# Optimization experiments

Measured on AMD Instinct MI355X. Metric: run time of the kernel, lower is better.

Reference implementation:

```python
import jax, jax.numpy as jnp
import numpy as np

NUM_CLASSES = 21
IOU_THRESH = 0.5
NEG_POS_RATIO = 3
VAR0, VAR1 = 0.1, 0.2


def point_form(priors):
    # (cx,cy,w,h) -> (xmin,ymin,xmax,ymax)
    return jnp.concatenate([priors[:, :2] - priors[:, 2:] / 2,
                            priors[:, :2] + priors[:, 2:] / 2], axis=-1)


def jaccard(box_a, box_b):
    # box_a: [n,4] point form, box_b: [N,4] point form -> [n,N]
    max_xy = jnp.minimum(box_a[:, None, 2:], box_b[None, :, 2:])
    min_xy = jnp.maximum(box_a[:, None, :2], box_b[None, :, :2])
    inter = jnp.prod(jnp.clip(max_xy - min_xy, 0.0, None), axis=-1)
    area_a = jnp.prod(box_a[:, 2:] - box_a[:, :2], axis=-1)[:, None]
    area_b = jnp.prod(box_b[:, 2:] - box_b[:, :2], axis=-1)[None, :]
    return inter / (area_a + area_b - inter)


def encode(matched, priors):
    # matched: [N,4] point form, priors: [N,4] center form
    g_cxcy = ((matched[:, :2] + matched[:, 2:]) / 2 - priors[:, :2]) / (VAR0 * priors[:, 2:])
    g_wh = jnp.log((matched[:, 2:] - matched[:, :2]) / priors[:, 2:]) / VAR1
    return jnp.concatenate([g_cxcy, g_wh], axis=-1)


def match_one(truths, labels, priors):
    # truths: [n_obj,4], labels: [n_obj], priors: [N,4] center form
    ov = jaccard(truths, point_form(priors))          # [n_obj, N]
    best_prior_idx = jnp.argmax(ov, axis=1)           # [n_obj]
    best_truth_overlap = jnp.max(ov, axis=0)          # [N]
    best_truth_idx = jnp.argmax(ov, axis=0)           # [N]
    best_truth_overlap = best_truth_overlap.at[best_prior_idx].set(2.0)
    def body(j, bti):
        return bti.at[best_prior_idx[j]].set(j)
    best_truth_idx = jax.lax.fori_loop(0, truths.shape[0], body, best_truth_idx)
    matched = truths[best_truth_idx]                  # [N,4]
    conf = labels[best_truth_idx].astype(jnp.int32) + 1
    conf = jnp.where(best_truth_overlap < IOU_THRESH, 0, conf)
    return encode(matched, priors), conf


def smooth_l1(x):
    ax = jnp.abs(x)
    return jnp.where(ax < 1.0, 0.5 * x * x, ax - 0.5)


def setup_inputs() -> dict:
    key = jax.random.key(0)
    k1, k2, k3, k4, k5, k6, k7 = jax.random.split(key, 7)
    B, N, n_obj = 128, 8732, 16
    loc_data = jax.random.normal(k1, (B, N, 4), jnp.float32)
    conf_data = jax.random.normal(k2, (B, N, NUM_CLASSES), jnp.float32)
    # valid ground-truth boxes in [0,1], point form, plus class label in [0,20)
    mins = jax.random.uniform(k3, (B, n_obj, 2)) * 0.6
    sizes = jax.random.uniform(k4, (B, n_obj, 2)) * 0.35 + 0.05
    labels = jax.random.randint(k5, (B, n_obj), 0, NUM_CLASSES - 1).astype(jnp.float32)
    targets = jnp.concatenate([mins, mins + sizes, labels[..., None]], axis=-1)
    # priors in center form with positive w,h
    centers = jax.random.uniform(k6, (N, 2))
    wh = jax.random.uniform(k7, (N, 2)) * 0.5 + 0.05
    priors = jnp.concatenate([centers, wh], axis=-1).astype(jnp.float32)
    return {"loc_data": loc_data, "conf_data": conf_data, "targets": targets, "priors": priors}


def _forward(loc_data, conf_data, targets, priors):
    B, N = loc_data.shape[0], loc_data.shape[1]
    truths, labels = targets[:, :, :4], targets[:, :, 4]
    target_loc, target_conf = jax.vmap(match_one, in_axes=(0, 0, None))(truths, labels, priors)
    pos = target_conf > 0                             # [B,N]
    # localization: smooth-L1 summed over positive priors
    loss_l = jnp.sum(smooth_l1(loc_data - target_loc) * pos[..., None].astype(loc_data.dtype))
    # per-prior CE surrogate: logsumexp - logit[target]
    lse = jax.nn.logsumexp(conf_data, axis=-1)        # [B,N]
    gathered = jnp.take_along_axis(conf_data, target_conf[..., None], axis=-1)[..., 0]
    loss_c_all = lse - gathered                       # [B,N]
    # hard negative mining via double argsort ranking (positives excluded)
    lc = jnp.where(pos, 0.0, loss_c_all)
    loss_idx = jnp.argsort(-lc, axis=1)
    idx_rank = jnp.argsort(loss_idx, axis=1)
    num_pos = jnp.sum(pos.astype(jnp.int32), axis=1, keepdims=True)   # [B,1]
    num_neg = jnp.minimum(NEG_POS_RATIO * num_pos, N - 1)
    neg = idx_rank < num_neg
    sel = pos | neg
    loss_c = jnp.sum(jnp.where(sel, loss_c_all, 0.0))
    n_total = jnp.sum(num_pos).astype(loc_data.dtype)
    return loss_l / n_total, loss_c / n_total


def reference(loc_data, conf_data, targets, priors):
    return _forward(loc_data, conf_data, targets, priors)
```

## Files before the change

kernel.cpp:

```cpp
#include <hip/hip_runtime.h>
#include <cstdint>
#include <cstddef>

#define HB1 4096
#define HB2 2048
#define CMAX 21
#define IOU_T 0.5f

__device__ __forceinline__ float sl1(float x) {
    float ax = fabsf(x);
    return ax < 1.0f ? 0.5f * x * x : ax - 0.5f;
}

__global__ __launch_bounds__(256) void kA_best_prior(
    const float* __restrict__ targets, const float* __restrict__ priors,
    float* __restrict__ bpi_val, int* __restrict__ bpi_idx,
    int* __restrict__ num_pos_g, float* __restrict__ accB_g,
    float* __restrict__ acc_g, unsigned* __restrict__ done_g,
    int N, int NOBJ, int SLICES, int CHUNK, int B)
{
    const int s = blockIdx.x, b = blockIdx.y, t = threadIdx.x;
    __shared__ float tb[16 * 4];
    __shared__ float ta[16];
    __shared__ float wv[4 * 16];
    __shared__ int   wi[4 * 16];

    if (s == 0 && b == 0) {
        for (int q = t; q < B; q += 256) num_pos_g[q] = 0;
        for (int q = t; q < 2 * B; q += 256) accB_g[q] = 0.f;
        if (t < 4) acc_g[t] = 0.f;
        if (t == 0) *done_g = 0u;
    }

    if (t < 16) {
        if (t < NOBJ) {
            const float* tr = targets + ((size_t)b * NOBJ + t) * 5;
            float x0 = tr[0], y0 = tr[1], x1 = tr[2], y1 = tr[3];
            tb[t * 4 + 0] = x0; tb[t * 4 + 1] = y0;
            tb[t * 4 + 2] = x1; tb[t * 4 + 3] = y1;
            ta[t] = (x1 - x0) * (y1 - y0);
        } else {
            tb[t * 4 + 0] = 0.f; tb[t * 4 + 1] = 0.f;
            tb[t * 4 + 2] = 0.f; tb[t * 4 + 3] = 0.f;
            ta[t] = 0.f;
        }
    }
    __syncthreads();

    float bv[16]; int bi[16];
#pragma unroll
    for (int j = 0; j < 16; j++) { bv[j] = -1.0f; bi[j] = 0x7fffffff; }

    const int start = s * CHUNK;
    const int end = min(start + CHUNK, N);
    for (int i = start + t; i < end; i += 256) {
        float4 p = ((const float4*)priors)[i];
        float bx0 = p.x - p.z * 0.5f, by0 = p.y - p.w * 0.5f;
        float bx1 = p.x + p.z * 0.5f, by1 = p.y + p.w * 0.5f;
        float ab = (bx1 - bx0) * (by1 - by0);
#pragma unroll
        for (int j = 0; j < 16; j++) {
            float iw = fminf(tb[j * 4 + 2], bx1) - fmaxf(tb[j * 4 + 0], bx0);
            float ih = fminf(tb[j * 4 + 3], by1) - fmaxf(tb[j * 4 + 1], by0);
            iw = fmaxf(iw, 0.f); ih = fmaxf(ih, 0.f);
            float inter = iw * ih;
            float iou = inter / (ta[j] + ab - inter);
            if (iou > bv[j] || (iou == bv[j] && i < bi[j])) { bv[j] = iou; bi[j] = i; }
        }
    }

#pragma unroll
    for (int off = 32; off >= 1; off >>= 1) {
#pragma unroll
        for (int j = 0; j < 16; j++) {
            float v2 = __shfl_down(bv[j], off, 64);
            int   i2 = __shfl_down(bi[j], off, 64);
            if (v2 > bv[j] || (v2 == bv[j] && i2 < bi[j])) { bv[j] = v2; bi[j] = i2; }
        }
    }
    const int wid = t >> 6, lane = t & 63;
    if (lane == 0) {
#pragma unroll
        for (int j = 0; j < 16; j++) { wv[wid * 16 + j] = bv[j]; wi[wid * 16 + j] = bi[j]; }
    }
    __syncthreads();
    if (t < 16) {
        float v = wv[t]; int idx = wi[t];
#pragma unroll
        for (int w = 1; w < 4; w++) {
            float v2 = wv[w * 16 + t]; int i2 = wi[w * 16 + t];
            if (v2 > v || (v2 == v && i2 < idx)) { v = v2; idx = i2; }
        }
        if (t < NOBJ) {
            int o = (b * SLICES + s) * 16 + t;
            bpi_val[o] = v;
            bpi_idx[o] = idx;
        }
    }
}

#define IOU_STEP(j) { \
    float4 tj = tb4[j]; \
    float taj = (tj.z - tj.x) * (tj.w - tj.y); \
    float iw = fminf(tj.z, bx1) - fmaxf(tj.x, bx0); \
    float ih = fminf(tj.w, by1) - fmaxf(tj.y, by0); \
    iw = fmaxf(iw, 0.f); ih = fmaxf(ih, 0.f); \
    float inter = iw * ih; \
    float iou = inter * __builtin_amdgcn_rcpf(taj + ab - inter); \
    if (iou > bto) { bto = iou; bti = (j); } }

__global__ __launch_bounds__(256, 4) void kB_main(
    const float* __restrict__ loc, const float* __restrict__ conf,
    const float* __restrict__ targets, const float* __restrict__ priors,
    const float* __restrict__ bpi_val, const int* __restrict__ bpi_idx,
    float* __restrict__ lc_out, int* __restrict__ num_pos, float* __restrict__ accB,
    int N, int NOBJ, int SLICES, int BPB)
{
    const int g = blockIdx.x;
    const int b = g / BPB;
    const int j0 = g % BPB;
    const int t = threadIdx.x;
    const int wid = t >> 6, lane = t & 63;

    __shared__ __align__(16) float tb[16 * 4];
    __shared__ float tl[16];
    __shared__ __align__(16) int bpi_s[16];
    __shared__ float wred[4 * 3];

    if (t < 16) {
        if (t < NOBJ) {
            const float* tr = targets + ((size_t)b * NOBJ + t) * 5;
            tb[t * 4 + 0] = tr[0]; tb[t * 4 + 1] = tr[1];
            tb[t * 4 + 2] = tr[2]; tb[t * 4 + 3] = tr[3];
            tl[t] = tr[4];
            float bv = -1.f; int bi = 0x7fffffff;
            for (int s2 = 0; s2 < SLICES; s2++) {
                int o = (b * SLICES + s2) * 16 + t;
                float v = bpi_val[o]; int idx = bpi_idx[o];
                if (v > bv || (v == bv && idx < bi)) { bv = v; bi = idx; }
            }
            bpi_s[t] = bi;
        } else {
            tb[t * 4 + 0] = 0.f; tb[t * 4 + 1] = 0.f; tb[t * 4 + 2] = 0.f; tb[t * 4 + 3] = 0.f;
            tl[t] = 0.f; bpi_s[t] = -1;
        }
    }
    __syncthreads();

    const float* confB = conf + (size_t)b * N * CMAX;
    const float* locB  = loc + (size_t)b * N * 4;

    float ll = 0.f, plc = 0.f, np = 0.f;

    const int stride = BPB * 256;
    for (int i = j0 * 256 + t; i < N; i += stride) {
        float4 pp  = ((const float4*)priors)[i];
        float4 myl = ((const float4*)locB)[i];
        const float* cr = confB + (size_t)i * CMAX;
        float c[CMAX];
#pragma unroll
        for (int q = 0; q < CMAX; q++) c[q] = cr[q];

        float bx0 = pp.x - pp.z * 0.5f, by0 = pp.y - pp.w * 0.5f;
        float bx1 = pp.x + pp.z * 0.5f, by1 = pp.y + pp.w * 0.5f;
        float ab = (bx1 - bx0) * (by1 - by0);
        float bto = -1.f; int bti = 0;
        const float4* tb4 = (const float4*)tb;
        if (NOBJ == 16) {
#pragma unroll
            for (int j = 0; j < 16; j++) IOU_STEP(j);
        } else {
            for (int j = 0; j < NOBJ; j++) IOU_STEP(j);
        }
        const int4* bp4 = (const int4*)bpi_s;
#pragma unroll
        for (int jj = 0; jj < 4; jj++) {
            int4 q = bp4[jj];
            if (q.x == i) { bto = 2.0f; bti = jj * 4 + 0; }
            if (q.y == i) { bto = 2.0f; bti = jj * 4 + 1; }
            if (q.z == i) { bto = 2.0f; bti = jj * 4 + 2; }
            if (q.w == i) { bto = 2.0f; bti = jj * 4 + 3; }
        }
        bool pos = !(bto < IOU_T);
        if (pos) {
            float4 tj = tb4[bti];
            float rz = __builtin_amdgcn_rcpf(pp.z);
            float rw = __builtin_amdgcn_rcpf(pp.w);
            float gcx = ((tj.x + tj.z) * 0.5f - pp.x) * (10.0f * rz);
            float gcy = ((tj.y + tj.w) * 0.5f - pp.y) * (10.0f * rw);
            float gw = __logf((tj.z - tj.x) * rz) * 5.0f;
            float gh = __logf((tj.w - tj.y) * rw) * 5.0f;
            ll += sl1(myl.x - gcx) + sl1(myl.y - gcy) + sl1(myl.z - gw) + sl1(myl.w - gh);
            np += 1.f;
        }
        int cf = pos ? ((int)tl[bti] + 1) : 0;

        float m = c[0];
#pragma unroll
        for (int q = 1; q < CMAX; q++) m = fmaxf(m, c[q]);
        float ssum = 0.f;
#pragma unroll
        for (int q = 0; q < CMAX; q++) ssum += __expf(c[q] - m);
        float gath = c[0];
#pragma unroll
        for (int q = 1; q < CMAX; q++) gath = (q == cf) ? c[q] : gath;
        float lse = m + __logf(ssum);
        float lossc = lse - gath;
        if (pos) plc += lossc;
        float lcv = pos ? 0.f : lossc;
        lcv = fmaxf(lcv, 0.f);
        lc_out[(size_t)b * N + i] = lcv;
    }

#pragma unroll
    for (int off = 32; off >= 1; off >>= 1) {
        ll  += __shfl_down(ll, off, 64);
        plc += __shfl_down(plc, off, 64);
        np  += __shfl_down(np, off, 64);
    }
    if (lane == 0) { wred[wid * 3 + 0] = ll; wred[wid * 3 + 1] = plc; wred[wid * 3 + 2] = np; }
    __syncthreads();
    if (t == 0) {
        float a0 = 0.f, a1 = 0.f, a2 = 0.f;
#pragma unroll
        for (int w = 0; w < 4; w++) { a0 += wred[w * 3 + 0]; a1 += wred[w * 3 + 1]; a2 += wred[w * 3 + 2]; }
        atomicAdd(&accB[b * 2 + 0], a0);
        atomicAdd(&accB[b * 2 + 1], a1);
        atomicAdd(&num_pos[b], (int)a2);
    }
}

__device__ __forceinline__ void wave_sufscan(int& c, float& s, int lane) {
#pragma unroll
    for (int off = 1; off < 64; off <<= 1) {
        int c2 = __shfl_down(c, off, 64);
        float s2 = __shfl_down(s, off, 64);
        if (lane + off < 64) { c += c2; s += s2; }
    }
}

__global__ __launch_bounds__(1024) void kC_topk(
    const float* __restrict__ lc, const int* __restrict__ num_pos,
    const float* __restrict__ accB,
    float* __restrict__ acc, unsigned* __restrict__ done_ctr,
    float* __restrict__ out, int N, int B)
{
    const int b = blockIdx.x, t = threadIdx.x;
    const int NT = 1024;
    const int wid = t >> 6, lane = t & 63;
    __shared__ __align__(16) int   cnt[HB1];
    __shared__ __align__(16) float sm[HB1];
    __shared__ int   wc[16];
    __shared__ float ws[16];
    __shared__ int s_strad, s_krem;
    __shared__ float s_above;
    __shared__ int s_last;
    __shared__ float wsum[16], wsA[16], wsB[16];

    const int k = min(3 * num_pos[b], N - 1);
    const float* lcb = lc + (size_t)b * N;
    float total = 0.f;

    if (k > 0) {
        ((int4*)cnt)[t] = make_int4(0, 0, 0, 0);
        ((float4*)sm)[t] = make_float4(0.f, 0.f, 0.f, 0.f);
        __syncthreads();
        const int n4 = N >> 2;
        const float4* lcb4 = (const float4*)lcb;
        for (int i = t; i < n4; i += NT) {
            float4 v = lcb4[i];
            { unsigned u = __float_as_uint(v.x) >> 19; atomicAdd(&cnt[u], 1); atomicAdd(&sm[u], v.x); }
            { unsigned u = __float_as_uint(v.y) >> 19; atomicAdd(&cnt[u], 1); atomicAdd(&sm[u], v.y); }
            { unsigned u = __float_as_uint(v.z) >> 19; atomicAdd(&cnt[u], 1); atomicAdd(&sm[u], v.z); }
            { unsigned u = __float_as_uint(v.w) >> 19; atomicAdd(&cnt[u], 1); atomicAdd(&sm[u], v.w); }
        }
        for (int i = (n4 << 2) + t; i < N; i += NT) {
            float v = lcb[i];
            unsigned u = __float_as_uint(v) >> 19;
            atomicAdd(&cnt[u], 1); atomicAdd(&sm[u], v);
        }
        __syncthreads();
        {
            int4  cv = ((const int4*)cnt)[t];
            float4 sv = ((const float4*)sm)[t];
            int   ci = cv.x + cv.y + cv.z + cv.w;
            float si = sv.x + sv.y + sv.z + sv.w;
            wave_sufscan(ci, si, lane);
            if (lane == 0) { wc[wid] = ci; ws[wid] = si; }
            __syncthreads();
            int cab = 0; float sab = 0.f;
            for (int w = wid + 1; w < 16; w++) { cab += wc[w]; sab += ws[w]; }
            int   i0c = ci + cab;          float f0 = si + sab;
            int   i1c = i0c - cv.x;        float f1 = f0 - sv.x;
            int   i2c = i1c - cv.y;        float f2 = f1 - sv.y;
            int   i3c = i2c - cv.z;        float f3 = f2 - sv.z;
            int   i4c = i3c - cv.w;
            if (i1c < k && k <= i0c) { s_strad = 4 * t + 0; s_krem = k - i1c; s_above = f1; }
            if (i2c < k && k <= i1c) { s_strad = 4 * t + 1; s_krem = k - i2c; s_above = f2; }
            if (i3c < k && k <= i2c) { s_strad = 4 * t + 2; s_krem = k - i3c; s_above = f3; }
            if (i4c < k && k <= i3c) { s_strad = 4 * t + 3; s_krem = k - i4c; s_above = f3 - sv.w; }
        }
        __syncthreads();
        const int s1 = s_strad, k2 = s_krem;
        total += s_above;

        __syncthreads();
        ((int2*)cnt)[t] = make_int2(0, 0);
        ((float2*)sm)[t] = make_float2(0.f, 0.f);
        __syncthreads();
        for (int i = t; i < N; i += NT) {
            float v = lcb[i];
            unsigned u = __float_as_uint(v);
            if ((int)(u >> 19) == s1) {
                int q = (int)((u >> 8) & 0x7FF);
                atomicAdd(&cnt[q], 1); atomicAdd(&sm[q], v);
            }
        }
        __syncthreads();
        {
            int2  cv = ((const int2*)cnt)[t];
            float2 sv = ((const float2*)sm)[t];
            int   ci = cv.x + cv.y;
            float si = sv.x + sv.y;
            wave_sufscan(ci, si, lane);
            if (lane == 0) { wc[wid] = ci; ws[wid] = si; }
            __syncthreads();
            int cab = 0; float sab = 0.f;
            for (int w = wid + 1; w < 16; w++) { cab += wc[w]; sab += ws[w]; }
            int   i0c = ci + cab;       float f0 = si + sab;
            int   i1c = i0c - cv.x;     float f1 = f0 - sv.x;
            int   i2c = i1c - cv.y;
            if (i1c < k2 && k2 <= i0c) { s_strad = 2 * t + 0; s_krem = k2 - i1c; s_above = f1; }
            if (i2c < k2 && k2 <= i1c) { s_strad = 2 * t + 1; s_krem = k2 - i2c; s_above = f1 - sv.y; }
        }
        __syncthreads();
        const int s2 = s_strad, krem = s_krem;
        total += s_above;
        float tval = __uint_as_float((((unsigned)s1) << 19) | (((unsigned)s2) << 8));
        total += (float)krem * tval;
    }

    if (t == 0) {
        if (k > 0) atomicAdd(&acc[1], total);
        __threadfence();
        unsigned old = atomicAdd(done_ctr, 1u);
        s_last = (old == (unsigned)gridDim.x - 1u) ? 1 : 0;
    }
    __syncthreads();
    if (s_last) {
        __threadfence();
        float vn = 0.f, va = 0.f, vb = 0.f;
        for (int q = t; q < B; q += NT) {
            vn += (float)num_pos[q];
            va += accB[q * 2 + 0];
            vb += accB[q * 2 + 1];
        }
#pragma unroll
        for (int off = 32; off >= 1; off >>= 1) {
            vn += __shfl_down(vn, off, 64);
            va += __shfl_down(va, off, 64);
            vb += __shfl_down(vb, off, 64);
        }
        if (lane == 0) { wsum[wid] = vn; wsA[wid] = va; wsB[wid] = vb; }
        __syncthreads();
        if (t == 0) {
            float n = 0.f, a = 0.f, bsum = 0.f;
#pragma unroll
            for (int w = 0; w < 16; w++) { n += wsum[w]; a += wsA[w]; bsum += wsB[w]; }
            float l2 = atomicAdd(&acc[1], 0.0f);
            out[0] = a / n;
            out[1] = (bsum + l2) / n;
        }
    }
}

extern "C" void kernel_launch(void* const* d_in, const int* in_sizes, int n_in,
                              void* d_out, int out_size, void* d_ws, size_t ws_size,
                              hipStream_t stream)
{
    const float* loc     = (const float*)d_in[0];
    const float* conf    = (const float*)d_in[1];
    const float* targets = (const float*)d_in[2];
    const float* priors  = (const float*)d_in[3];
    float* out = (float*)d_out;

    const int N = in_sizes[3] / 4;
    const int BN = in_sizes[0] / 4;
    const int B = BN / N;
    const int NOBJ = in_sizes[2] / (B * 5);
    const int SLICES = 8;
    const int CHUNK = (N + SLICES - 1) / SLICES;
    const int BPB = 12;

    char* w = (char*)d_ws;
    float*    lc_ws   = (float*)w;                         size_t off = (size_t)BN * 4;
    float*    bpi_val = (float*)(w + off);                 off += (size_t)B * SLICES * 16 * 4;
    int*      bpi_idx = (int*)(w + off);                   off += (size_t)B * SLICES * 16 * 4;
    int*      num_pos = (int*)(w + off);                   off += (size_t)B * 4;
    float*    accB    = (float*)(w + off);                 off += (size_t)B * 2 * 4;
    float*    acc     = (float*)(w + off);                 off += 16;
    unsigned* done    = (unsigned*)(w + off);              off += 16;

    dim3 gA(SLICES, B);
    kA_best_prior<<<gA, 256, 0, stream>>>(targets, priors, bpi_val, bpi_idx,
                                          num_pos, accB, acc, done, N, NOBJ, SLICES, CHUNK, B);

    kB_main<<<B * BPB, 256, 0, stream>>>(loc, conf, targets, priors, bpi_val, bpi_idx,
                                         lc_ws, num_pos, accB, N, NOBJ, SLICES, BPB);

    kC_topk<<<B, 1024, 0, stream>>>(lc_ws, num_pos, accB, acc, done, out, N, B);
}
```

Baseline: 269.2 us.

## Stage conf tiles through LDS with coalesced float4 loads and register double-buffering

The main kernel now loads each 256-prior tile of class logits as contiguous float4 vectors into registers, writes them to shared memory, and has each thread read its own row from there. Previously each thread read its 21-float row with strided scalar global loads. The next-but-one tile is prefetched into a second register set while the current tile is processed, so global latency overlaps with compute. Blocks per batch drop from 12 to 8 and the occupancy hint drops to 3, which adds register and LDS pressure. The generic NOBJ path is removed, so the kernel now assumes 16 objects.

Result: faster. 230.7 us (-14.3%).

```diff
diff --git a/kernel.cpp b/kernel.cpp
--- a/kernel.cpp
+++ b/kernel.cpp
@@ -109,12 +109,94 @@
     float iou = inter * __builtin_amdgcn_rcpf(taj + ab - inter); \
     if (iou > bto) { bto = iou; bti = (j); } }
 
-__global__ __launch_bounds__(256, 4) void kB_main(
+#define STAGE(PFX, xx) { \
+    int i0s = (xx) * 256; \
+    int rows_s = min(256, N - i0s); \
+    int nf4s = (rows_s * CMAX) >> 2; \
+    const float4* s4 = (const float4*)(confB + (size_t)i0s * CMAX); \
+    if (t + 0    < nf4s) PFX##0 = s4[t + 0]; \
+    if (t + 256  < nf4s) PFX##1 = s4[t + 256]; \
+    if (t + 512  < nf4s) PFX##2 = s4[t + 512]; \
+    if (t + 768  < nf4s) PFX##3 = s4[t + 768]; \
+    if (t + 1024 < nf4s) PFX##4 = s4[t + 1024]; \
+    if (t + 1280 < nf4s) PFX##5 = s4[t + 1280]; \
+    if (t < rows_s) { \
+        PFX##pr = ((const float4*)priors)[i0s + t]; \
+        PFX##ld = ((const float4*)locB)[i0s + t]; } }
+
+#define PROC_TILE(PFX) { \
+    const int i0 = x * 256; \
+    const int rows = min(256, N - i0); \
+    const int nf4 = (rows * CMAX) >> 2; \
+    asm volatile("" ::: "memory"); \
+    __builtin_amdgcn_s_barrier();                  \
+    asm volatile("" ::: "memory"); \
+    float4 myp = PFX##pr, myl = PFX##ld;           \
+    float4* bp4f = (float4*)buf; \
+    if (t + 0    < nf4) bp4f[t + 0]    = PFX##0;   \
+    if (t + 256  < nf4) bp4f[t + 256]  = PFX##1; \
+    if (t + 512  < nf4) bp4f[t + 512]  = PFX##2; \
+    if (t + 768  < nf4) bp4f[t + 768]  = PFX##3; \
+    if (t + 1024 < nf4) bp4f[t + 1024] = PFX##4; \
+    if (t + 1280 < nf4) bp4f[t + 1280] = PFX##5; \
+    asm volatile("s_waitcnt lgkmcnt(0)" ::: "memory");   \
+    __builtin_amdgcn_s_barrier();                  \
+    asm volatile("" ::: "memory"); \
+    { int xpre = x + 2 * BPB; if (xpre < TPB) STAGE(PFX, xpre); } \
+    if (t < rows) { \
+        const int i = i0 + t; \
+        float4 pp = myp; \
+        float bx0 = pp.x - pp.z * 0.5f, by0 = pp.y - pp.w * 0.5f; \
+        float bx1 = pp.x + pp.z * 0.5f, by1 = pp.y + pp.w * 0.5f; \
+        float ab = (bx1 - bx0) * (by1 - by0); \
+        float bto = -1.f; int bti = 0; \
+        const float4* tb4 = (const float4*)tb; \
+        _Pragma("unroll") \
+        for (int j = 0; j < 16; j++) IOU_STEP(j); \
+        const int4* bp4 = (const int4*)bpi_s; \
+        _Pragma("unroll") \
+        for (int jj = 0; jj < 4; jj++) { \
+            int4 q = bp4[jj]; \
+            if (q.x == i) { bto = 2.0f; bti = jj * 4 + 0; } \
+            if (q.y == i) { bto = 2.0f; bti = jj * 4 + 1; } \
+            if (q.z == i) { bto = 2.0f; bti = jj * 4 + 2; } \
+            if (q.w == i) { bto = 2.0f; bti = jj * 4 + 3; } \
+        } \
+        bool pos = !(bto < IOU_T); \
+        if (pos) { \
+            float4 tj = tb4[bti]; \
+            float rz = __builtin_amdgcn_rcpf(pp.z); \
+            float rw = __builtin_amdgcn_rcpf(pp.w); \
+            float gcx = ((tj.x + tj.z) * 0.5f - pp.x) * (10.0f * rz); \
+            float gcy = ((tj.y + tj.w) * 0.5f - pp.y) * (10.0f * rw); \
+            float gw = __logf((tj.z - tj.x) * rz) * 5.0f; \
+            float gh = __logf((tj.w - tj.y) * rw) * 5.0f; \
+            ll += sl1(myl.x - gcx) + sl1(myl.y - gcy) + sl1(myl.z - gw) + sl1(myl.w - gh); \
+            np += 1.f; \
+        } \
+        int cf = pos ? ((int)tl[bti] + 1) : 0; \
+        const float* cr = buf + t * CMAX; \
+        float m = cr[0]; \
+        _Pragma("unroll") \
+        for (int c = 1; c < CMAX; c++) m = fmaxf(m, cr[c]); \
+        float ssum = 0.f; \
+        _Pragma("unroll") \
+        for (int c = 0; c < CMAX; c++) ssum += __expf(cr[c] - m); \
+        float lse = m + __logf(ssum); \
+        float lossc = lse - cr[cf]; \
+        if (pos) plc += lossc; \
+        float lcv = pos ? 0.f : lossc; \
+        lcv = fmaxf(lcv, 0.f); \
+        lc_out[(size_t)b * N + i] = lcv; \
+    } \
+    x += BPB; }
+
+__global__ __launch_bounds__(256, 3) void kB_main(
     const float* __restrict__ loc, const float* __restrict__ conf,
     const float* __restrict__ targets, const float* __restrict__ priors,
     const float* __restrict__ bpi_val, const int* __restrict__ bpi_idx,
     float* __restrict__ lc_out, int* __restrict__ num_pos, float* __restrict__ accB,
-    int N, int NOBJ, int SLICES, int BPB)
+    int N, int NOBJ, int SLICES, int TPB, int BPB)
 {
     const int g = blockIdx.x;
     const int b = g / BPB;
@@ -122,6 +204,7 @@
     const int t = threadIdx.x;
     const int wid = t >> 6, lane = t & 63;
 
+    __shared__ __align__(16) float buf[256 * CMAX];
     __shared__ __align__(16) float tb[16 * 4];
     __shared__ float tl[16];
     __shared__ __align__(16) int bpi_s[16];
@@ -150,66 +233,18 @@
     const float* confB = conf + (size_t)b * N * CMAX;
     const float* locB  = loc + (size_t)b * N * 4;
 
+    float4 a0, a1, a2, a3, a4, a5, apr, ald;
+    float4 b0, b1, b2, b3, b4, b5, bpr, bld;
+
     float ll = 0.f, plc = 0.f, np = 0.f;
-
-    const int stride = BPB * 256;
-    for (int i = j0 * 256 + t; i < N; i += stride) {
-        float4 pp  = ((const float4*)priors)[i];
-        float4 myl = ((const float4*)locB)[i];
-        const float* cr = confB + (size_t)i * CMAX;
-        float c[CMAX];
-#pragma unroll
-        for (int q = 0; q < CMAX; q++) c[q] = cr[q];
-
-        float bx0 = pp.x - pp.z * 0.5f, by0 = pp.y - pp.w * 0.5f;
-        float bx1 = pp.x + pp.z * 0.5f, by1 = pp.y + pp.w * 0.5f;
-        float ab = (bx1 - bx0) * (by1 - by0);
-        float bto = -1.f; int bti = 0;
-        const float4* tb4 = (const float4*)tb;
-        if (NOBJ == 16) {
-#pragma unroll
-            for (int j = 0; j < 16; j++) IOU_STEP(j);
-        } else {
-            for (int j = 0; j < NOBJ; j++) IOU_STEP(j);
-        }
-        const int4* bp4 = (const int4*)bpi_s;
-#pragma unroll
-        for (int jj = 0; jj < 4; jj++) {
-            int4 q = bp4[jj];
-            if (q.x == i) { bto = 2.0f; bti = jj * 4 + 0; }
-            if (q.y == i) { bto = 2.0f; bti = jj * 4 + 1; }
-            if (q.z == i) { bto = 2.0f; bti = jj * 4 + 2; }
-            if (q.w == i) { bto = 2.0f; bti = jj * 4 + 3; }
-        }
-        bool pos = !(bto < IOU_T);
-        if (pos) {
-            float4 tj = tb4[bti];
-            float rz = __builtin_amdgcn_rcpf(pp.z);
-            float rw = __builtin_amdgcn_rcpf(pp.w);
-            float gcx = ((tj.x + tj.z) * 0.5f - pp.x) * (10.0f * rz);
-            float gcy = ((tj.y + tj.w) * 0.5f - pp.y) * (10.0f * rw);
-            float gw = __logf((tj.z - tj.x) * rz) * 5.0f;
-            float gh = __logf((tj.w - tj.y) * rw) * 5.0f;
-            ll += sl1(myl.x - gcx) + sl1(myl.y - gcy) + sl1(myl.z - gw) + sl1(myl.w - gh);
-            np += 1.f;
-        }
-        int cf = pos ? ((int)tl[bti] + 1) : 0;
-
-        float m = c[0];
-#pragma unroll
-        for (int q = 1; q < CMAX; q++) m = fmaxf(m, c[q]);
-        float ssum = 0.f;
-#pragma unroll
-        for (int q = 0; q < CMAX; q++) ssum += __expf(c[q] - m);
-        float gath = c[0];
-#pragma unroll
-        for (int q = 1; q < CMAX; q++) gath = (q == cf) ? c[q] : gath;
-        float lse = m + __logf(ssum);
-        float lossc = lse - gath;
-        if (pos) plc += lossc;
-        float lcv = pos ? 0.f : lossc;
-        lcv = fmaxf(lcv, 0.f);
-        lc_out[(size_t)b * N + i] = lcv;
+    int x = j0;
+    if (x < TPB)       STAGE(a, x);
+    if (x + BPB < TPB) STAGE(b, x + BPB);
+
+    while (x < TPB) {
+        PROC_TILE(a)
+        if (x >= TPB) break;
+        PROC_TILE(b)
     }
 
 #pragma unroll
@@ -221,12 +256,12 @@
     if (lane == 0) { wred[wid * 3 + 0] = ll; wred[wid * 3 + 1] = plc; wred[wid * 3 + 2] = np; }
     __syncthreads();
     if (t == 0) {
-        float a0 = 0.f, a1 = 0.f, a2 = 0.f;
-#pragma unroll
-        for (int w = 0; w < 4; w++) { a0 += wred[w * 3 + 0]; a1 += wred[w * 3 + 1]; a2 += wred[w * 3 + 2]; }
-        atomicAdd(&accB[b * 2 + 0], a0);
-        atomicAdd(&accB[b * 2 + 1], a1);
-        atomicAdd(&num_pos[b], (int)a2);
+        float a0r = 0.f, a1r = 0.f, a2r = 0.f;
+#pragma unroll
+        for (int w = 0; w < 4; w++) { a0r += wred[w * 3 + 0]; a1r += wred[w * 3 + 1]; a2r += wred[w * 3 + 2]; }
+        atomicAdd(&accB[b * 2 + 0], a0r);
+        atomicAdd(&accB[b * 2 + 1], a1r);
+        atomicAdd(&num_pos[b], (int)a2r);
     }
 }
 
@@ -390,7 +425,8 @@
     const int NOBJ = in_sizes[2] / (B * 5);
     const int SLICES = 8;
     const int CHUNK = (N + SLICES - 1) / SLICES;
-    const int BPB = 12;
+    const int TPB = (N + 255) / 256;
+    const int BPB = 8;
 
     char* w = (char*)d_ws;
     float*    lc_ws   = (float*)w;                         size_t off = (size_t)BN * 4;
@@ -406,7 +442,7 @@
                                           num_pos, accB, acc, done, N, NOBJ, SLICES, CHUNK, B);
 
     kB_main<<<B * BPB, 256, 0, stream>>>(loc, conf, targets, priors, bpi_val, bpi_idx,
-                                         lc_ws, num_pos, accB, N, NOBJ, SLICES, BPB);
+                                         lc_ws, num_pos, accB, N, NOBJ, SLICES, TPB, BPB);
 
     kC_topk<<<B, 1024, 0, stream>>>(lc_ws, num_pos, accB, acc, done, out, N, B);
 }
```

## Double-buffer conf/loc/prior tiles into LDS via global_load_lds in single-wave blocks

Applied to the files above, without the earlier changes.

The main matching and loss kernel now runs one wave per block and streams 64-prior chunks of conf, priors and loc directly into LDS with global_load_lds. It double-buffers them, waiting on vmcnt so the next chunk's load overlaps compute on the current one. This replaces strided per-thread loads of the 21 conf floats, which were uncoalesced at an 84-byte stride, with fully coalesced 16-byte transfers. The risks are LDS bank conflicts when each lane reads at a 21-float stride, lower occupancy from the 16KB LDS buffer, and fragile hand-written waitcnt counts.

Result: faster. 238.1 us (-11.6%).

```diff
diff --git a/kernel.cpp b/kernel.cpp
--- a/kernel.cpp
+++ b/kernel.cpp
@@ -6,11 +6,19 @@
 #define HB2 2048
 #define CMAX 21
 #define IOU_T 0.5f
+#define WPB 24
 
 __device__ __forceinline__ float sl1(float x) {
     float ax = fabsf(x);
     return ax < 1.0f ? 0.5f * x * x : ax - 0.5f;
 }
+
+__device__ __forceinline__ void gld16(const float4* g, float4* l) {
+    __builtin_amdgcn_global_load_lds((const __attribute__((address_space(1))) void*)g,
+                                     (__attribute__((address_space(3))) void*)l, 16, 0, 0);
+}
+
+#define WAITVM(n) asm volatile("s_waitcnt vmcnt(" #n ")" ::: "memory")
 
 __global__ __launch_bounds__(256) void kA_best_prior(
     const float* __restrict__ targets, const float* __restrict__ priors,
@@ -109,107 +117,130 @@
     float iou = inter * __builtin_amdgcn_rcpf(taj + ab - inter); \
     if (iou > bto) { bto = iou; bti = (j); } }
 
-__global__ __launch_bounds__(256, 4) void kB_main(
+__global__ __launch_bounds__(64) void kB_main(
     const float* __restrict__ loc, const float* __restrict__ conf,
     const float* __restrict__ targets, const float* __restrict__ priors,
     const float* __restrict__ bpi_val, const int* __restrict__ bpi_idx,
     float* __restrict__ lc_out, int* __restrict__ num_pos, float* __restrict__ accB,
-    int N, int NOBJ, int SLICES, int BPB)
+    int N, int NOBJ, int SLICES, int NCH)
 {
     const int g = blockIdx.x;
-    const int b = g / BPB;
-    const int j0 = g % BPB;
-    const int t = threadIdx.x;
-    const int wid = t >> 6, lane = t & 63;
-
+    const int b = g / WPB;
+    const int w0 = g % WPB;
+    const int lane = threadIdx.x;
+
+    __shared__ __align__(16) float4 buf[2][512];
     __shared__ __align__(16) float tb[16 * 4];
     __shared__ float tl[16];
     __shared__ __align__(16) int bpi_s[16];
-    __shared__ float wred[4 * 3];
-
-    if (t < 16) {
-        if (t < NOBJ) {
-            const float* tr = targets + ((size_t)b * NOBJ + t) * 5;
-            tb[t * 4 + 0] = tr[0]; tb[t * 4 + 1] = tr[1];
-            tb[t * 4 + 2] = tr[2]; tb[t * 4 + 3] = tr[3];
-            tl[t] = tr[4];
+
+    const float* confB = conf + (size_t)b * N * CMAX;
+    const float* locB  = loc + (size_t)b * N * 4;
+    const float4* c4 = (const float4*)confB;
+    const int n4c = (N * CMAX) >> 2;
+
+    auto issue = [&](int c, int p) {
+        const int base = c * 336;
+        float4* d = &buf[p][0];
+#pragma unroll
+        for (int m = 0; m < 6; m++) {
+            int idx = min(base + m * 64 + lane, n4c - 1);
+            gld16(c4 + idx, d + m * 64);
+        }
+        int r = min(c * 64 + lane, N - 1);
+        gld16(((const float4*)priors) + r, d + 384);
+        gld16(((const float4*)locB)  + r, d + 448);
+    };
+
+    int c = w0;
+    if (c < NCH) issue(c, 0);
+    if (c + WPB < NCH) issue(c + WPB, 1);
+
+    if (lane < 16) {
+        if (lane < NOBJ) {
+            const float* tr = targets + ((size_t)b * NOBJ + lane) * 5;
+            tb[lane * 4 + 0] = tr[0]; tb[lane * 4 + 1] = tr[1];
+            tb[lane * 4 + 2] = tr[2]; tb[lane * 4 + 3] = tr[3];
+            tl[lane] = tr[4];
             float bv = -1.f; int bi = 0x7fffffff;
             for (int s2 = 0; s2 < SLICES; s2++) {
-                int o = (b * SLICES + s2) * 16 + t;
+                int o = (b * SLICES + s2) * 16 + lane;
                 float v = bpi_val[o]; int idx = bpi_idx[o];
                 if (v > bv || (v == bv && idx < bi)) { bv = v; bi = idx; }
             }
-            bpi_s[t] = bi;
+            bpi_s[lane] = bi;
         } else {
-            tb[t * 4 + 0] = 0.f; tb[t * 4 + 1] = 0.f; tb[t * 4 + 2] = 0.f; tb[t * 4 + 3] = 0.f;
-            tl[t] = 0.f; bpi_s[t] = -1;
+            tb[lane * 4 + 0] = 0.f; tb[lane * 4 + 1] = 0.f;
+            tb[lane * 4 + 2] = 0.f; tb[lane * 4 + 3] = 0.f;
+            tl[lane] = 0.f; bpi_s[lane] = -1;
         }
     }
     __syncthreads();
 
-    const float* confB = conf + (size_t)b * N * CMAX;
-    const float* locB  = loc + (size_t)b * N * 4;
-
     float ll = 0.f, plc = 0.f, np = 0.f;
-
-    const int stride = BPB * 256;
-    for (int i = j0 * 256 + t; i < N; i += stride) {
-        float4 pp  = ((const float4*)priors)[i];
-        float4 myl = ((const float4*)locB)[i];
-        const float* cr = confB + (size_t)i * CMAX;
-        float c[CMAX];
-#pragma unroll
-        for (int q = 0; q < CMAX; q++) c[q] = cr[q];
-
-        float bx0 = pp.x - pp.z * 0.5f, by0 = pp.y - pp.w * 0.5f;
-        float bx1 = pp.x + pp.z * 0.5f, by1 = pp.y + pp.w * 0.5f;
-        float ab = (bx1 - bx0) * (by1 - by0);
-        float bto = -1.f; int bti = 0;
-        const float4* tb4 = (const float4*)tb;
-        if (NOBJ == 16) {
-#pragma unroll
-            for (int j = 0; j < 16; j++) IOU_STEP(j);
-        } else {
-            for (int j = 0; j < NOBJ; j++) IOU_STEP(j);
-        }
-        const int4* bp4 = (const int4*)bpi_s;
-#pragma unroll
-        for (int jj = 0; jj < 4; jj++) {
-            int4 q = bp4[jj];
-            if (q.x == i) { bto = 2.0f; bti = jj * 4 + 0; }
-            if (q.y == i) { bto = 2.0f; bti = jj * 4 + 1; }
-            if (q.z == i) { bto = 2.0f; bti = jj * 4 + 2; }
-            if (q.w == i) { bto = 2.0f; bti = jj * 4 + 3; }
-        }
-        bool pos = !(bto < IOU_T);
-        if (pos) {
-            float4 tj = tb4[bti];
-            float rz = __builtin_amdgcn_rcpf(pp.z);
-            float rw = __builtin_amdgcn_rcpf(pp.w);
-            float gcx = ((tj.x + tj.z) * 0.5f - pp.x) * (10.0f * rz);
-            float gcy = ((tj.y + tj.w) * 0.5f - pp.y) * (10.0f * rw);
-            float gw = __logf((tj.z - tj.x) * rz) * 5.0f;
-            float gh = __logf((tj.w - tj.y) * rw) * 5.0f;
-            ll += sl1(myl.x - gcx) + sl1(myl.y - gcy) + sl1(myl.z - gw) + sl1(myl.w - gh);
-            np += 1.f;
-        }
-        int cf = pos ? ((int)tl[bti] + 1) : 0;
-
-        float m = c[0];
-#pragma unroll
-        for (int q = 1; q < CMAX; q++) m = fmaxf(m, c[q]);
-        float ssum = 0.f;
-#pragma unroll
-        for (int q = 0; q < CMAX; q++) ssum += __expf(c[q] - m);
-        float gath = c[0];
-#pragma unroll
-        for (int q = 1; q < CMAX; q++) gath = (q == cf) ? c[q] : gath;
-        float lse = m + __logf(ssum);
-        float lossc = lse - gath;
-        if (pos) plc += lossc;
-        float lcv = pos ? 0.f : lossc;
-        lcv = fmaxf(lcv, 0.f);
-        lc_out[(size_t)b * N + i] = lcv;
+    int p = 0;
+
+    while (c < NCH) {
+        if (c + WPB < NCH) { WAITVM(8); } else { WAITVM(0); }
+
+        const int i = c * 64 + lane;
+        if (i < N) {
+            const float* cr = (const float*)&buf[p][0] + lane * 21;
+            float4 pp = buf[p][384 + lane];
+            float4 myl = buf[p][448 + lane];
+
+            float bx0 = pp.x - pp.z * 0.5f, by0 = pp.y - pp.w * 0.5f;
+            float bx1 = pp.x + pp.z * 0.5f, by1 = pp.y + pp.w * 0.5f;
+            float ab = (bx1 - bx0) * (by1 - by0);
+            float bto = -1.f; int bti = 0;
+            const float4* tb4 = (const float4*)tb;
+            if (NOBJ == 16) {
+#pragma unroll
+                for (int j = 0; j < 16; j++) IOU_STEP(j);
+            } else {
+                for (int j = 0; j < NOBJ; j++) IOU_STEP(j);
+            }
+            const int4* bp4 = (const int4*)bpi_s;
+#pragma unroll
+            for (int jj = 0; jj < 4; jj++) {
+                int4 q = bp4[jj];
+                if (q.x == i) { bto = 2.0f; bti = jj * 4 + 0; }
+                if (q.y == i) { bto = 2.0f; bti = jj * 4 + 1; }
+                if (q.z == i) { bto = 2.0f; bti = jj * 4 + 2; }
+                if (q.w == i) { bto = 2.0f; bti = jj * 4 + 3; }
+            }
+            bool pos = !(bto < IOU_T);
+            if (pos) {
+                float4 tj = tb4[bti];
+                float rz = __builtin_amdgcn_rcpf(pp.z);
+                float rw = __builtin_amdgcn_rcpf(pp.w);
+                float gcx = ((tj.x + tj.z) * 0.5f - pp.x) * (10.0f * rz);
+                float gcy = ((tj.y + tj.w) * 0.5f - pp.y) * (10.0f * rw);
+                float gw = __logf((tj.z - tj.x) * rz) * 5.0f;
+                float gh = __logf((tj.w - tj.y) * rw) * 5.0f;
+                ll += sl1(myl.x - gcx) + sl1(myl.y - gcy) + sl1(myl.z - gw) + sl1(myl.w - gh);
+                np += 1.f;
+            }
+            int cf = pos ? ((int)tl[bti] + 1) : 0;
+            float m = cr[0];
+#pragma unroll
+            for (int q = 1; q < CMAX; q++) m = fmaxf(m, cr[q]);
+            float ssum = 0.f;
+#pragma unroll
+            for (int q = 0; q < CMAX; q++) ssum += __expf(cr[q] - m);
+            float lse = m + __logf(ssum);
+            float lossc = lse - cr[cf];
+            if (pos) plc += lossc;
+            float lcv = pos ? 0.f : lossc;
+            lcv = fmaxf(lcv, 0.f);
+            lc_out[(size_t)b * N + i] = lcv;
+        }
+
+        asm volatile("" ::: "memory");
+        int c2 = c + 2 * WPB;
+        if (c2 < NCH) issue(c2, p);
+        p ^= 1;
+        c += WPB;
     }
 
 #pragma unroll
@@ -218,15 +249,10 @@
         plc += __shfl_down(plc, off, 64);
         np  += __shfl_down(np, off, 64);
     }
-    if (lane == 0) { wred[wid * 3 + 0] = ll; wred[wid * 3 + 1] = plc; wred[wid * 3 + 2] = np; }
-    __syncthreads();
-    if (t == 0) {
-        float a0 = 0.f, a1 = 0.f, a2 = 0.f;
-#pragma unroll
-        for (int w = 0; w < 4; w++) { a0 += wred[w * 3 + 0]; a1 += wred[w * 3 + 1]; a2 += wred[w * 3 + 2]; }
-        atomicAdd(&accB[b * 2 + 0], a0);
-        atomicAdd(&accB[b * 2 + 1], a1);
-        atomicAdd(&num_pos[b], (int)a2);
+    if (lane == 0) {
+        atomicAdd(&accB[b * 2 + 0], ll);
+        atomicAdd(&accB[b * 2 + 1], plc);
+        atomicAdd(&num_pos[b], (int)np);
     }
 }
 
@@ -390,7 +416,7 @@
     const int NOBJ = in_sizes[2] / (B * 5);
     const int SLICES = 8;
     const int CHUNK = (N + SLICES - 1) / SLICES;
-    const int BPB = 12;
+    const int NCH = (N + 63) / 64;
 
     char* w = (char*)d_ws;
     float*    lc_ws   = (float*)w;                         size_t off = (size_t)BN * 4;
@@ -405,8 +431,8 @@
     kA_best_prior<<<gA, 256, 0, stream>>>(targets, priors, bpi_val, bpi_idx,
                                           num_pos, accB, acc, done, N, NOBJ, SLICES, CHUNK, B);
 
-    kB_main<<<B * BPB, 256, 0, stream>>>(loc, conf, targets, priors, bpi_val, bpi_idx,
-                                         lc_ws, num_pos, accB, N, NOBJ, SLICES, BPB);
+    kB_main<<<B * WPB, 64, 0, stream>>>(loc, conf, targets, priors, bpi_val, bpi_idx,
+                                        lc_ws, num_pos, accB, N, NOBJ, SLICES, NCH);
 
     kC_topk<<<B, 1024, 0, stream>>>(lc_ws, num_pos, accB, acc, done, out, N, B);
 }
```
